# Kernel tuning notes

Measured on AMD Instinct MI355X. Metric: run time of the kernel, lower is better.

Reference implementation:

```python
import jax, jax.numpy as jnp
import numpy as np

NPOINT = 2048
RADII = (0.4, 0.8)
NSAMPLES = (16, 32)
EPS = 1e-5


def _fps(xyz, npoint):
    # iterative farthest point sampling, start at index 0 (matches CUDA kernel)
    B, N, _ = xyz.shape

    def step(carry, _):
        dist, last = carry  # dist [B,N], last [B]
        lx = jnp.take_along_axis(xyz, last[:, None, None], axis=1)  # [B,1,3]
        d = jnp.sum((xyz - lx) ** 2, axis=-1)  # [B,N]
        dist = jnp.minimum(dist, d)
        nxt = jnp.argmax(dist, axis=1).astype(jnp.int32)
        return (dist, nxt), last

    init = (jnp.full((B, N), 1e10, xyz.dtype), jnp.zeros((B,), jnp.int32))
    _, idxs = jax.lax.scan(step, init, None, length=npoint)
    return idxs.T  # [B, npoint]


def _ball_query(radius, nsample, xyz, new_xyz):
    # first-nsample points within radius, in original order; pad with first hit (0 if none)
    N = xyz.shape[1]
    d2 = jnp.sum((new_xyz[:, :, None, :] - xyz[:, None, :, :]) ** 2, axis=-1)  # [B,S,N]
    mask = d2 < radius * radius
    ar = jnp.arange(N, dtype=jnp.int32)
    key = jnp.where(mask, ar, N + ar)  # in-range first, stable original order
    order = jnp.argsort(key, axis=-1)[..., :nsample].astype(jnp.int32)  # [B,S,ns]
    cnt = mask.sum(axis=-1, keepdims=True)  # [B,S,1]
    valid = jnp.arange(nsample) < cnt
    return jnp.where(valid, order, order[..., :1])


def _bn_relu(x):
    # training-mode BatchNorm (gamma=1, beta=0) over all dims but channel (last)
    red = tuple(range(x.ndim - 1))
    mu = x.mean(axis=red, keepdims=True)
    var = x.var(axis=red, keepdims=True)
    return jax.nn.relu((x - mu) * jax.lax.rsqrt(var + EPS))


def _scale(xyz, new_xyz, feats, radius, nsample, ws):
    idx = _ball_query(radius, nsample, xyz, new_xyz)  # [B,S,ns]
    B, S, ns = idx.shape
    flat = idx.reshape(B, S * ns)
    gx = jnp.take_along_axis(xyz, flat[..., None], axis=1).reshape(B, S, ns, 3)
    gx = gx - new_xyz[:, :, None, :]  # relative coords
    gf = jnp.take_along_axis(feats, flat[..., None], axis=1).reshape(B, S, ns, -1)
    h = jnp.concatenate([gx, gf], axis=-1)  # [B,S,ns,3+C]
    for w in ws:
        h = _bn_relu(h @ w)  # pointwise conv (kernel 1) + BN + ReLU
    return h.max(axis=2)  # max-pool over group -> [B,S,Cout]


def setup_inputs() -> dict:
    key = jax.random.key(0)
    ks = jax.random.split(key, 16)
    s = 0.02
    return {
        "xyz": jax.random.normal(ks[0], (8, 8192, 3), jnp.float32),
        "features": jax.random.normal(ks[1], (8, 8192, 64), jnp.float32),
        "w0_0": jax.random.normal(ks[2], (67, 64), jnp.float32) * s,
        "w0_1": jax.random.normal(ks[3], (64, 64), jnp.float32) * s,
        "w0_2": jax.random.normal(ks[4], (64, 128), jnp.float32) * s,
        "w1_0": jax.random.normal(ks[5], (67, 64), jnp.float32) * s,
        "w1_1": jax.random.normal(ks[6], (64, 64), jnp.float32) * s,
        "w1_2": jax.random.normal(ks[7], (64, 128), jnp.float32) * s,
        "agg_w": jax.random.normal(ks[8], (256, 256), jnp.float32) * s,
        "agg_b": jax.random.normal(ks[9], (256,), jnp.float32) * s,
        "conf_w": jax.random.normal(ks[10], (256, 256), jnp.float32) * s,
        "cls_w": jax.random.normal(ks[11], (256, 3), jnp.float32) * s,
        "cls_b": jax.random.normal(ks[12], (3,), jnp.float32) * s,
    }


def reference(xyz, features, w0_0, w0_1, w0_2, w1_0, w1_1, w1_2,
              agg_w, agg_b, conf_w, cls_w, cls_b):
    idx = _fps(xyz, NPOINT)  # [B,S]
    new_xyz = jnp.take_along_axis(xyz, idx[..., None], axis=1)  # [B,S,3]
    f0 = _scale(xyz, new_xyz, features, RADII[0], NSAMPLES[0], (w0_0, w0_1, w0_2))
    f1 = _scale(xyz, new_xyz, features, RADII[1], NSAMPLES[1], (w1_0, w1_1, w1_2))
    h = jnp.concatenate([f0, f1], axis=-1)  # [B,S,256]
    h = _bn_relu(h @ agg_w + agg_b)  # aggregation Linear + BN + ReLU
    c = _bn_relu(h @ conf_w)  # confidence hidden layer
    cls = c @ cls_w + cls_b  # [B,S,num_class]
    return new_xyz, h, cls
```

## Files before the change

kernel.cpp:

```cpp
#include <hip/hip_runtime.h>
#include <cstdint>
#include <cstddef>

constexpr int Bb = 8;
constexpr int Nn = 8192;
constexpr int Ss = 2048;
constexpr int BS = Bb * Ss;

typedef float vfloat2 __attribute__((ext_vector_type(2)));

__global__ __launch_bounds__(1024) void fps_kernel(const float* __restrict__ xyz,
                                                   float* __restrict__ new_xyz) {
  __shared__ float lx[Nn * 3];
  __shared__ int sidx[Ss];
  __shared__ unsigned long long slotV[2];
  __shared__ int slotI[2];
  const int b = blockIdx.x;
  const int tid = threadIdx.x;
  const float* xb = xyz + (size_t)b * Nn * 3;
  for (int e = tid; e < Nn * 3; e += 1024) lx[e] = xb[e];
  if (tid == 0) {
    slotV[0] = 0ull; slotV[1] = 0ull;
    slotI[0] = 0x7fffffff; slotI[1] = 0x7fffffff;
  }
  __syncthreads();

  vfloat2 px2[4], py2[4], pz2[4], df2[4];
  double dist[8];
#pragma unroll
  for (int jj = 0; jj < 4; ++jj) {
    const int p0 = tid + (2 * jj) * 1024, p1 = tid + (2 * jj + 1) * 1024;
    px2[jj] = (vfloat2){lx[p0 * 3 + 0], lx[p1 * 3 + 0]};
    py2[jj] = (vfloat2){lx[p0 * 3 + 1], lx[p1 * 3 + 1]};
    pz2[jj] = (vfloat2){lx[p0 * 3 + 2], lx[p1 * 3 + 2]};
    df2[jj] = (vfloat2){3.0e38f, 3.0e38f};
    dist[2 * jj] = 1e10;
    dist[2 * jj + 1] = 1e10;
  }
  float lmax = 3.0e38f;
  int cur = 0;
  double lv = -1.0;
  int li = 0x7fffffff;
  float lv32 = -1.0f;
  float wv32_c = -1.0f;
  for (int i = 0; i < Ss; ++i) {
    if (tid == 0) sidx[i] = cur;
    const float cxf = lx[cur * 3 + 0], cyf = lx[cur * 3 + 1], czf = lx[cur * 3 + 2];
    const vfloat2 cx2 = {cxf, cxf}, cy2 = {cyf, cyf}, cz2 = {czf, czf};
    const bool wasTop = (lv32 == wv32_c);
    vfloat2 d2v[4];
#pragma unroll
    for (int jj = 0; jj < 4; ++jj) {
      const vfloat2 dx = px2[jj] - cx2;
      const vfloat2 dy = py2[jj] - cy2;
      const vfloat2 dz = pz2[jj] - cz2;
      d2v[jj] = dx * dx + dy * dy + dz * dz;
    }
    const float dmin = fminf(fminf(fminf(d2v[0].x, d2v[0].y), fminf(d2v[1].x, d2v[1].y)),
                             fminf(fminf(d2v[2].x, d2v[2].y), fminf(d2v[3].x, d2v[3].y)));
    bool changed = false;
    if (dmin <= lmax) {
#pragma unroll
      for (int j = 0; j < 8; ++j) {
        const float d2s = d2v[j >> 1][j & 1];
        const float dfs = (j & 1) ? df2[j >> 1].y : df2[j >> 1].x;
        if (d2s <= dfs) {
          const float pxs = px2[j >> 1][j & 1];
          const float pys = py2[j >> 1][j & 1];
          const float pzs = pz2[j >> 1][j & 1];
          double dx = __dsub_rn((double)pxs, (double)cxf);
          double dy = __dsub_rn((double)pys, (double)cyf);
          double dz = __dsub_rn((double)pzs, (double)czf);
          double d = __dadd_rn(__dadd_rn(__dmul_rn(dx, dx), __dmul_rn(dy, dy)),
                               __dmul_rn(dz, dz));
          if (d < dist[j]) {
            dist[j] = d;
            const float dfn = (float)d * 1.000002f;
            if (j & 1) df2[j >> 1].y = dfn; else df2[j >> 1].x = dfn;
            changed = true;
          }
        }
      }
      if (changed) {
        lv = -1.0;
        li = 0;
#pragma unroll
        for (int j = 0; j < 8; ++j) {
          if (dist[j] > lv) { lv = dist[j]; li = tid + j * 1024; }
        }
        lv32 = (float)lv;
        lmax = fmaxf(fmaxf(fmaxf(df2[0].x, df2[0].y), fmaxf(df2[1].x, df2[1].y)),
                     fmaxf(fmaxf(df2[2].x, df2[2].y), fmaxf(df2[3].x, df2[3].y)));
      }
    }
    const unsigned long long topChanged = __ballot(changed && wasTop);
    if (topChanged) {
      float m32 = lv32;
#pragma unroll
      for (int off = 1; off < 64; off <<= 1) m32 = fmaxf(m32, __shfl_xor(m32, off));
      wv32_c = m32;
    }
    const int pb = i & 1;
    if (lv32 == wv32_c) atomicMax(&slotV[pb], (unsigned long long)__double_as_longlong(lv));
    __syncthreads();
    const double W = __longlong_as_double((long long)slotV[pb]);
    if (lv == W) atomicMin(&slotI[pb], li);
    if (tid == 0) {
      slotV[pb ^ 1] = 0ull;
      slotI[pb ^ 1] = 0x7fffffff;
    }
    __syncthreads();
    cur = slotI[pb];
  }
  __syncthreads();
  float* nxb = new_xyz + (size_t)b * Ss * 3;
  for (int e = tid; e < Ss * 3; e += 1024) {
    const int i = e / 3, c = e - i * 3;
    nxb[e] = lx[sidx[i] * 3 + c];
  }
}

__global__ __launch_bounds__(256) void ballq_kernel(const float* __restrict__ xyz,
                                                    const float* __restrict__ nxyz,
                                                    int* __restrict__ idx0,
                                                    int* __restrict__ idx1) {
  const int wid = threadIdx.x >> 6, lane = threadIdx.x & 63;
  const int bs = blockIdx.x * 4 + wid;
  const int b = bs >> 11;
  const float* xb = xyz + (size_t)b * Nn * 3;
  const double cx = (double)nxyz[bs * 3 + 0];
  const double cy = (double)nxyz[bs * 3 + 1];
  const double cz = (double)nxyz[bs * 3 + 2];
  const double R0 = 0.4 * 0.4, R1 = 0.8 * 0.8;
  int cnt0 = 0, cnt1 = 0, first0 = 0, first1 = 0;
  const unsigned long long lmask = (1ull << lane) - 1ull;
  for (int base = 0; base < Nn; base += 64) {
    const int p = base + lane;
    double dx = __dsub_rn((double)xb[p * 3 + 0], cx);
    double dy = __dsub_rn((double)xb[p * 3 + 1], cy);
    double dz = __dsub_rn((double)xb[p * 3 + 2], cz);
    double d2 = __dadd_rn(__dadd_rn(__dmul_rn(dx, dx), __dmul_rn(dy, dy)), __dmul_rn(dz, dz));
    const bool in0 = d2 < R0, in1 = d2 < R1;
    unsigned long long m0 = __ballot(in0);
    unsigned long long m1 = __ballot(in1);
    if (cnt0 < 16 && m0) {
      if (cnt0 == 0) first0 = base + __builtin_ctzll(m0);
      int r = (int)__popcll(m0 & lmask);
      if (in0 && cnt0 + r < 16) idx0[bs * 16 + cnt0 + r] = p;
      cnt0 += (int)__popcll(m0);
    }
    if (cnt1 < 32 && m1) {
      if (cnt1 == 0) first1 = base + __builtin_ctzll(m1);
      int r = (int)__popcll(m1 & lmask);
      if (in1 && cnt1 + r < 32) idx1[bs * 32 + cnt1 + r] = p;
      cnt1 += (int)__popcll(m1);
    }
    if (cnt0 >= 16 && cnt1 >= 32) break;
  }
  const int f0 = cnt0 < 16 ? cnt0 : 16;
  for (int j = f0 + lane; j < 16; j += 64) idx0[bs * 16 + j] = first0;
  const int f1 = cnt1 < 32 ? cnt1 : 32;
  for (int j = f1 + lane; j < 32; j += 64) idx1[bs * 32 + j] = first1;
}

template <int COUT, int KTOT, int MODE, int NS, bool POOL, bool BIAS>
__global__ __launch_bounds__(256) void mlp_gemm(
    const float* __restrict__ xin, const float* __restrict__ xin2,
    const float* __restrict__ stIn, const float* __restrict__ stIn2,
    float invM1, float invM2,
    const float* __restrict__ w, const float* __restrict__ bias,
    const int* __restrict__ gidx, const float* __restrict__ xyz,
    const float* __restrict__ nxyz, const float* __restrict__ feats,
    float* __restrict__ hw, float* __restrict__ out, float* __restrict__ Sout) {
  constexpr int KC = (KTOT <= 68) ? KTOT : 32;
  constexpr int NCH = (KTOT + KC - 1) / KC;
  constexpr int TC = COUT / 16;
  constexpr int XPAD = KC + 1;
  constexpr int XSZ = 64 * XPAD;
  constexpr int EPI = (POOL ? 48 : 32) * COUT;
  constexpr int SM = (XSZ + KC * COUT > EPI) ? (XSZ + KC * COUT) : EPI;
  constexpr int BNSZ = (MODE == 0) ? 0 : 512;
  __shared__ float smem[SM + BNSZ];
  float* xS = smem;
  float* wS = smem + XSZ;
  float* bnM = smem + SM;
  float* bnR = smem + SM + 256;

  const int tid = threadIdx.x;
  const int cg = tid & 15, rg = tid >> 4;
  const int row0 = blockIdx.x * 64;

  if constexpr (MODE != 0) {
    for (int c = tid; c < KTOT; c += 256) {
      float sum, sq, im;
      if constexpr (MODE == 2) {
        if (c < 128) { sum = stIn[c]; sq = stIn[128 + c]; im = invM1; }
        else { sum = stIn2[c - 128]; sq = stIn2[c]; im = invM2; }
      } else {
        constexpr int C = (MODE == 1) ? 64 : 256;
        sum = stIn[c]; sq = stIn[C + c]; im = invM1;
      }
      const float mu = sum * im;
      const float var = sq * im - mu * mu;
      bnM[c] = mu;
      bnR[c] = 1.0f / sqrtf(var + 1e-5f);
    }
    __syncthreads();
  }

  float acc[4][TC];
#pragma unroll
  for (int i = 0; i < 4; ++i)
#pragma unroll
    for (int t = 0; t < TC; ++t) acc[i][t] = 0.f;

  for (int ch = 0; ch < NCH; ++ch) {
    const int k0 = ch * KC;
    if (ch) __syncthreads();
    for (int e = tid; e < 64 * KC; e += 256) {
      const int r = e / KC, kk = e - r * KC;
      const int kg = k0 + kk;
      const int rowg = row0 + r;
      float v;
      if constexpr (MODE == 0) {
        const int bs = rowg / NS;
        const int p = gidx[rowg];
        const int bb = bs >> 11;
        if (kg < 3)
          v = xyz[(bb * Nn + p) * 3 + kg] - nxyz[bs * 3 + kg];
        else
          v = feats[((bb * Nn + p) << 6) + (kg - 3)];
      } else if constexpr (MODE == 1) {
        v = fmaxf((xin[(size_t)rowg * 64 + kg] - bnM[kg]) * bnR[kg], 0.f);
      } else if constexpr (MODE == 2) {
        if (kg < 128)
          v = fmaxf((xin[(size_t)rowg * 128 + kg] - bnM[kg]) * bnR[kg], 0.f);
        else
          v = fmaxf((xin2[(size_t)rowg * 128 + (kg - 128)] - bnM[kg]) * bnR[kg], 0.f);
      } else {
        v = fmaxf((xin[(size_t)rowg * 256 + kg] - bnM[kg]) * bnR[kg], 0.f);
        hw[(size_t)rowg * 256 + kg] = v;
      }
      xS[r * XPAD + kk] = v;
    }
    for (int e = tid; e < KC * COUT; e += 256) {
      const int kk = e / COUT, c = e - kk * COUT;
      wS[kk * COUT + c] = w[(size_t)(k0 + kk) * COUT + c];
    }
    __syncthreads();
    for (int kk = 0; kk < KC; ++kk) {
      float xr[4];
#pragma unroll
      for (int i = 0; i < 4; ++i) xr[i] = xS[(rg * 4 + i) * XPAD + kk];
#pragma unroll
      for (int t = 0; t < TC; t += 4) {
        const float4 wv = *(const float4*)&wS[kk * COUT + cg * TC + t];
#pragma unroll
        for (int i = 0; i < 4; ++i) {
          acc[i][t + 0] = fmaf(xr[i], wv.x, acc[i][t + 0]);
          acc[i][t + 1] = fmaf(xr[i], wv.y, acc[i][t + 1]);
          acc[i][t + 2] = fmaf(xr[i], wv.z, acc[i][t + 2]);
          acc[i][t + 3] = fmaf(xr[i], wv.w, acc[i][t + 3]);
        }
      }
    }
  }
  __syncthreads();
  if constexpr (BIAS) {
#pragma unroll
    for (int t = 0; t < TC; ++t) {
      const float bv = bias[cg * TC + t];
#pragma unroll
      for (int i = 0; i < 4; ++i) acc[i][t] += bv;
    }
  }
  float* ssum = smem;
  float* ssq = smem + 16 * COUT;
  float* pbuf = smem + 32 * COUT;
  const int colb = cg * TC;
#pragma unroll
  for (int t = 0; t < TC; ++t) {
    float s = 0.f, q = 0.f, m = -3.4e38f;
#pragma unroll
    for (int i = 0; i < 4; ++i) {
      const float v = acc[i][t];
      s += v;
      q = fmaf(v, v, q);
      m = fmaxf(m, v);
    }
    ssum[rg * COUT + colb + t] = s;
    ssq[rg * COUT + colb + t] = q;
    if constexpr (POOL) pbuf[rg * COUT + colb + t] = m;
  }
  __syncthreads();
  for (int c = tid; c < COUT; c += 256) {
    float s = 0.f, q = 0.f;
#pragma unroll
    for (int rr = 0; rr < 16; ++rr) {
      s += ssum[rr * COUT + c];
      q += ssq[rr * COUT + c];
    }
    atomicAdd(&Sout[c], s);
    atomicAdd(&Sout[COUT + c], q);
  }
  if constexpr (POOL) {
    constexpr int G = 64 / NS, RPG = NS / 4;
    for (int o = tid; o < G * COUT; o += 256) {
      const int g = o / COUT, c = o - g * COUT;
      float m = pbuf[(g * RPG) * COUT + c];
#pragma unroll
      for (int qq = 1; qq < RPG; ++qq) m = fmaxf(m, pbuf[(g * RPG + qq) * COUT + c]);
      out[(size_t)(blockIdx.x * G + g) * COUT + c] = m;
    }
  } else {
#pragma unroll
    for (int i = 0; i < 4; ++i) {
      float* op = out + (size_t)(row0 + rg * 4 + i) * COUT + colb;
#pragma unroll
      for (int t = 0; t < TC; t += 4) {
        *(float4*)(op + t) = make_float4(acc[i][t], acc[i][t + 1], acc[i][t + 2], acc[i][t + 3]);
      }
    }
  }
}

__global__ __launch_bounds__(256) void cls_kernel(const float* __restrict__ craw,
                                                  const float* __restrict__ st,
                                                  const float* __restrict__ clsw,
                                                  const float* __restrict__ clsb,
                                                  float* __restrict__ outc) {
  __shared__ float bnM[256], bnR[256];
  const int tid = threadIdx.x;
  {
    const float im = 1.0f / 16384.0f;
    const float sum = st[tid], sq = st[256 + tid];
    const float mu = sum * im;
    const float var = sq * im - mu * mu;
    bnM[tid] = mu;
    bnR[tid] = 1.0f / sqrtf(var + 1e-5f);
  }
  __syncthreads();
  const int wid = tid >> 6, lane = tid & 63;
  const int row = blockIdx.x * 4 + wid;
  const float* cr = craw + (size_t)row * 256;
  float a0 = 0.f, a1 = 0.f, a2 = 0.f;
#pragma unroll 4
  for (int k = lane; k < 256; k += 64) {
    float x = fmaxf((cr[k] - bnM[k]) * bnR[k], 0.f);
    a0 = fmaf(x, clsw[k * 3 + 0], a0);
    a1 = fmaf(x, clsw[k * 3 + 1], a1);
    a2 = fmaf(x, clsw[k * 3 + 2], a2);
  }
#pragma unroll
  for (int off = 32; off; off >>= 1) {
    a0 += __shfl_down(a0, off);
    a1 += __shfl_down(a1, off);
    a2 += __shfl_down(a2, off);
  }
  if (lane == 0) {
    outc[row * 3 + 0] = a0 + clsb[0];
    outc[row * 3 + 1] = a1 + clsb[1];
    outc[row * 3 + 2] = a2 + clsb[2];
  }
}

extern "C" void kernel_launch(void* const* d_in, const int* in_sizes, int n_in,
                              void* d_out, int out_size, void* d_ws, size_t ws_size,
                              hipStream_t stream) {
  (void)in_sizes; (void)n_in; (void)out_size; (void)ws_size;
  const float* xyz = (const float*)d_in[0];
  const float* feats = (const float*)d_in[1];
  const float* w00 = (const float*)d_in[2];
  const float* w01 = (const float*)d_in[3];
  const float* w02 = (const float*)d_in[4];
  const float* w10 = (const float*)d_in[5];
  const float* w11 = (const float*)d_in[6];
  const float* w12 = (const float*)d_in[7];
  const float* aggw = (const float*)d_in[8];
  const float* aggb = (const float*)d_in[9];
  const float* confw = (const float*)d_in[10];
  const float* clsw = (const float*)d_in[11];
  const float* clsb = (const float*)d_in[12];

  float* outp = (float*)d_out;
  float* nxyz = outp;
  float* hout = outp + (size_t)BS * 3;
  float* clsout = hout + (size_t)BS * 256;

  char* ws = (char*)d_ws;
  const size_t MB = 1u << 20;
  int* idx0 = (int*)(ws + 0);
  int* idx1 = (int*)(ws + 1 * MB);
  float* st = (float*)(ws + 3 * MB);
  float* pool0 = (float*)(ws + 12 * MB);
  float* pool1 = (float*)(ws + 20 * MB);
  float* aggraw = (float*)(ws + 28 * MB);
  float* confraw = (float*)(ws + 44 * MB);
  float* hA = (float*)(ws + 60 * MB);

  hipMemsetAsync(st, 0, 2048 * sizeof(float), stream);

  const float iM0 = 1.0f / 262144.0f;
  const float iM1 = 1.0f / 524288.0f;
  const float iMh = 1.0f / 16384.0f;

  fps_kernel<<<Bb, 1024, 0, stream>>>(xyz, nxyz);
  ballq_kernel<<<BS / 4, 256, 0, stream>>>(xyz, nxyz, idx0, idx1);

  mlp_gemm<64, 67, 0, 16, false, false><<<4096, 256, 0, stream>>>(
      nullptr, nullptr, nullptr, nullptr, 0.f, 0.f, w00, nullptr,
      idx0, xyz, nxyz, feats, nullptr, hA, st + 0);
  mlp_gemm<64, 64, 1, 1, false, false><<<4096, 256, 0, stream>>>(
      hA, nullptr, st + 0, nullptr, iM0, 0.f, w01, nullptr,
      nullptr, nullptr, nullptr, nullptr, nullptr, hA, st + 128);
  mlp_gemm<128, 64, 1, 16, true, false><<<4096, 256, 0, stream>>>(
      hA, nullptr, st + 128, nullptr, iM0, 0.f, w02, nullptr,
      nullptr, nullptr, nullptr, nullptr, nullptr, pool0, st + 256);

  mlp_gemm<64, 67, 0, 32, false, false><<<8192, 256, 0, stream>>>(
      nullptr, nullptr, nullptr, nullptr, 0.f, 0.f, w10, nullptr,
      idx1, xyz, nxyz, feats, nullptr, hA, st + 512);
  mlp_gemm<64, 64, 1, 1, false, false><<<8192, 256, 0, stream>>>(
      hA, nullptr, st + 512, nullptr, iM1, 0.f, w11, nullptr,
      nullptr, nullptr, nullptr, nullptr, nullptr, hA, st + 640);
  mlp_gemm<128, 64, 1, 32, true, false><<<8192, 256, 0, stream>>>(
      hA, nullptr, st + 640, nullptr, iM1, 0.f, w12, nullptr,
      nullptr, nullptr, nullptr, nullptr, nullptr, pool1, st + 768);

  mlp_gemm<256, 256, 2, 1, false, true><<<256, 256, 0, stream>>>(
      pool0, pool1, st + 256, st + 768, iM0, iM1, aggw, aggb,
      nullptr, nullptr, nullptr, nullptr, nullptr, aggraw, st + 1024);

  mlp_gemm<256, 256, 4, 1, false, false><<<256, 256, 0, stream>>>(
      aggraw, nullptr, st + 1024, nullptr, iMh, 0.f, confw, nullptr,
      nullptr, nullptr, nullptr, nullptr, hout, confraw, st + 1536);

  cls_kernel<<<BS / 4, 256, 0, stream>>>(confraw, st + 1536, clsw, clsb, clsout);
}
```

Baseline: 3.959 ms.

## Spread BN-stat atomics over slots and use float ball-query with double fallback

```diff
diff --git a/kernel.cpp b/kernel.cpp
--- a/kernel.cpp
+++ b/kernel.cpp
@@ -6,6 +6,7 @@
 constexpr int Nn = 8192;
 constexpr int Ss = 2048;
 constexpr int BS = Bb * Ss;
+constexpr int NSL = 32;
 
 typedef float vfloat2 __attribute__((ext_vector_type(2)));
 
@@ -128,19 +129,38 @@
   const int bs = blockIdx.x * 4 + wid;
   const int b = bs >> 11;
   const float* xb = xyz + (size_t)b * Nn * 3;
-  const double cx = (double)nxyz[bs * 3 + 0];
-  const double cy = (double)nxyz[bs * 3 + 1];
-  const double cz = (double)nxyz[bs * 3 + 2];
-  const double R0 = 0.4 * 0.4, R1 = 0.8 * 0.8;
+  const float cxf = nxyz[bs * 3 + 0];
+  const float cyf = nxyz[bs * 3 + 1];
+  const float czf = nxyz[bs * 3 + 2];
+  const double R0d = 0.4 * 0.4, R1d = 0.8 * 0.8;
+  const float R0lo = 0.16f * (1.0f - 1e-5f), R0hi = 0.16f * (1.0f + 1e-5f);
+  const float R1lo = 0.64f * (1.0f - 1e-5f), R1hi = 0.64f * (1.0f + 1e-5f);
   int cnt0 = 0, cnt1 = 0, first0 = 0, first1 = 0;
   const unsigned long long lmask = (1ull << lane) - 1ull;
   for (int base = 0; base < Nn; base += 64) {
     const int p = base + lane;
-    double dx = __dsub_rn((double)xb[p * 3 + 0], cx);
-    double dy = __dsub_rn((double)xb[p * 3 + 1], cy);
-    double dz = __dsub_rn((double)xb[p * 3 + 2], cz);
-    double d2 = __dadd_rn(__dadd_rn(__dmul_rn(dx, dx), __dmul_rn(dy, dy)), __dmul_rn(dz, dz));
-    const bool in0 = d2 < R0, in1 = d2 < R1;
+    const float pxs = xb[p * 3 + 0], pys = xb[p * 3 + 1], pzs = xb[p * 3 + 2];
+    const float dxf = pxs - cxf, dyf = pys - cyf, dzf = pzs - czf;
+    const float d2f = fmaf(dxf, dxf, fmaf(dyf, dyf, dzf * dzf));
+    bool in0, in1;
+    if (d2f < R0lo) in0 = true;
+    else if (d2f > R0hi) in0 = false;
+    else {
+      double dx = __dsub_rn((double)pxs, (double)cxf);
+      double dy = __dsub_rn((double)pys, (double)cyf);
+      double dz = __dsub_rn((double)pzs, (double)czf);
+      double d2 = __dadd_rn(__dadd_rn(__dmul_rn(dx, dx), __dmul_rn(dy, dy)), __dmul_rn(dz, dz));
+      in0 = d2 < R0d;
+    }
+    if (d2f < R1lo) in1 = true;
+    else if (d2f > R1hi) in1 = false;
+    else {
+      double dx = __dsub_rn((double)pxs, (double)cxf);
+      double dy = __dsub_rn((double)pys, (double)cyf);
+      double dz = __dsub_rn((double)pzs, (double)czf);
+      double d2 = __dadd_rn(__dadd_rn(__dmul_rn(dx, dx), __dmul_rn(dy, dy)), __dmul_rn(dz, dz));
+      in1 = d2 < R1d;
+    }
     unsigned long long m0 = __ballot(in0);
     unsigned long long m1 = __ballot(in1);
     if (cnt0 < 16 && m0) {
@@ -192,13 +212,24 @@
 
   if constexpr (MODE != 0) {
     for (int c = tid; c < KTOT; c += 256) {
-      float sum, sq, im;
+      float sum = 0.f, sq = 0.f, im;
       if constexpr (MODE == 2) {
-        if (c < 128) { sum = stIn[c]; sq = stIn[128 + c]; im = invM1; }
-        else { sum = stIn2[c - 128]; sq = stIn2[c]; im = invM2; }
+        const float* base = (c < 128) ? stIn : stIn2;
+        const int cc = (c < 128) ? c : c - 128;
+        im = (c < 128) ? invM1 : invM2;
+#pragma unroll
+        for (int s = 0; s < NSL; ++s) {
+          sum += base[cc * NSL + s];
+          sq += base[(128 + cc) * NSL + s];
+        }
       } else {
         constexpr int C = (MODE == 1) ? 64 : 256;
-        sum = stIn[c]; sq = stIn[C + c]; im = invM1;
+        im = invM1;
+#pragma unroll
+        for (int s = 0; s < NSL; ++s) {
+          sum += stIn[c * NSL + s];
+          sq += stIn[(C + c) * NSL + s];
+        }
       }
       const float mu = sum * im;
       const float var = sq * im - mu * mu;
@@ -293,6 +324,7 @@
     if constexpr (POOL) pbuf[rg * COUT + colb + t] = m;
   }
   __syncthreads();
+  const int slot = blockIdx.x & (NSL - 1);
   for (int c = tid; c < COUT; c += 256) {
     float s = 0.f, q = 0.f;
 #pragma unroll
@@ -300,8 +332,8 @@
       s += ssum[rr * COUT + c];
       q += ssq[rr * COUT + c];
     }
-    atomicAdd(&Sout[c], s);
-    atomicAdd(&Sout[COUT + c], q);
+    atomicAdd(&Sout[c * NSL + slot], s);
+    atomicAdd(&Sout[(COUT + c) * NSL + slot], q);
   }
   if constexpr (POOL) {
     constexpr int G = 64 / NS, RPG = NS / 4;
@@ -332,8 +364,13 @@
   __shared__ float bnM[256], bnR[256];
   const int tid = threadIdx.x;
   {
+    float sum = 0.f, sq = 0.f;
+#pragma unroll
+    for (int s = 0; s < NSL; ++s) {
+      sum += st[tid * NSL + s];
+      sq += st[(256 + tid) * NSL + s];
+    }
     const float im = 1.0f / 16384.0f;
-    const float sum = st[tid], sq = st[256 + tid];
     const float mu = sum * im;
     const float var = sq * im - mu * mu;
     bnM[tid] = mu;
@@ -398,7 +435,7 @@
   float* confraw = (float*)(ws + 44 * MB);
   float* hA = (float*)(ws + 60 * MB);
 
-  hipMemsetAsync(st, 0, 2048 * sizeof(float), stream);
+  hipMemsetAsync(st, 0, 65536 * sizeof(float), stream);
 
   const float iM0 = 1.0f / 262144.0f;
   const float iM1 = 1.0f / 524288.0f;
@@ -412,28 +449,28 @@
       idx0, xyz, nxyz, feats, nullptr, hA, st + 0);
   mlp_gemm<64, 64, 1, 1, false, false><<<4096, 256, 0, stream>>>(
       hA, nullptr, st + 0, nullptr, iM0, 0.f, w01, nullptr,
-      nullptr, nullptr, nullptr, nullptr, nullptr, hA, st + 128);
+      nullptr, nullptr, nullptr, nullptr, nullptr, hA, st + 4096);
   mlp_gemm<128, 64, 1, 16, true, false><<<4096, 256, 0, stream>>>(
-      hA, nullptr, st + 128, nullptr, iM0, 0.f, w02, nullptr,
-      nullptr, nullptr, nullptr, nullptr, nullptr, pool0, st + 256);
+      hA, nullptr, st + 4096, nullptr, iM0, 0.f, w02, nullptr,
+      nullptr, nullptr, nullptr, nullptr, nullptr, pool0, st + 8192);
 
   mlp_gemm<64, 67, 0, 32, false, false><<<8192, 256, 0, stream>>>(
       nullptr, nullptr, nullptr, nullptr, 0.f, 0.f, w10, nullptr,
-      idx1, xyz, nxyz, feats, nullptr, hA, st + 512);
+      idx1, xyz, nxyz, feats, nullptr, hA, st + 16384);
   mlp_gemm<64, 64, 1, 1, false, false><<<8192, 256, 0, stream>>>(
-      hA, nullptr, st + 512, nullptr, iM1, 0.f, w11, nullptr,
-      nullptr, nullptr, nullptr, nullptr, nullptr, hA, st + 640);
+      hA, nullptr, st + 16384, nullptr, iM1, 0.f, w11, nullptr,
+      nullptr, nullptr, nullptr, nullptr, nullptr, hA, st + 20480);
   mlp_gemm<128, 64, 1, 32, true, false><<<8192, 256, 0, stream>>>(
-      hA, nullptr, st + 640, nullptr, iM1, 0.f, w12, nullptr,
-      nullptr, nullptr, nullptr, nullptr, nullptr, pool1, st + 768);
+      hA, nullptr, st + 20480, nullptr, iM1, 0.f, w12, nullptr,
+      nullptr, nullptr, nullptr, nullptr, nullptr, pool1, st + 24576);
 
   mlp_gemm<256, 256, 2, 1, false, true><<<256, 256, 0, stream>>>(
-      pool0, pool1, st + 256, st + 768, iM0, iM1, aggw, aggb,
-      nullptr, nullptr, nullptr, nullptr, nullptr, aggraw, st + 1024);
+      pool0, pool1, st + 8192, st + 24576, iM0, iM1, aggw, aggb,
+      nullptr, nullptr, nullptr, nullptr, nullptr, aggraw, st + 32768);
 
   mlp_gemm<256, 256, 4, 1, false, false><<<256, 256, 0, stream>>>(
-      aggraw, nullptr, st + 1024, nullptr, iMh, 0.f, confw, nullptr,
-      nullptr, nullptr, nullptr, nullptr, hout, confraw, st + 1536);
-
-  cls_kernel<<<BS / 4, 256, 0, stream>>>(confraw, st + 1536, clsw, clsb, clsout);
+      aggraw, nullptr, st + 32768, nullptr, iMh, 0.f, confw, nullptr,
+      nullptr, nullptr, nullptr, nullptr, hout, confraw, st + 49152);
+
+  cls_kernel<<<BS / 4, 256, 0, stream>>>(confraw, st + 49152, clsw, clsb, clsout);
 }
```

New measurement: 3.702 ms. -6.5%, faster.
